# Kernel tuning notes

Hardware: AMD Instinct MI355X
Metric: run time of the kernel (lower is better)

## Reference

```python
import jax, jax.numpy as jnp
import numpy as np

B, T, D, U, N = 32, 2048, 128, 512, 256
THETA = 1000.0


def _lmu_AT_BT(order, theta):
    # Legendre delay state-space (Voelker LMU), then ZOH discretization (dt=1).
    q = np.arange(order, dtype=np.float32)
    r = (2.0 * q + 1.0) / np.float32(theta)
    i, j = np.meshgrid(q, q, indexing='ij')
    A = np.where(i < j, -1.0, (-1.0) ** (i - j + 1)).astype(np.float32) * r[:, None]
    Bv = ((-1.0) ** q).astype(np.float32) * r
    # ZOH via augmented matrix exponential: expm([[A, B],[0, 0]])
    M = np.zeros((order + 1, order + 1), np.float32)
    M[:order, :order] = A
    M[:order, order] = Bv
    eM = jax.scipy.linalg.expm(jnp.asarray(M))
    Ad = eM[:order, :order]
    Bd = eM[:order, order:order + 1]
    AT = (Ad - jnp.eye(order, dtype=jnp.float32)).T  # (A_d - I)^T, [N,N]
    BT = Bd.T  # [1,N]
    return AT, BT


def setup_inputs() -> dict:
    key = jax.random.key(0)
    ks = jax.random.split(key, 6)
    AT, BT = _lmu_AT_BT(N, THETA)
    return {
        'x': jax.random.normal(ks[0], (B, T, D), jnp.float32),
        'h0': jnp.zeros((B, U), jnp.float32),
        'm0': jnp.zeros((B, N), jnp.float32),
        'input_encoders': jax.random.normal(ks[1], (D, 1), jnp.float32) / jnp.sqrt(jnp.float32(D)),
        'hidden_encoders': jax.random.normal(ks[2], (U, 1), jnp.float32) / jnp.sqrt(jnp.float32(U)),
        'memory_encoders': jnp.zeros((N, 1), jnp.float32),
        'input_kernel': jax.random.normal(ks[3], (D, U), jnp.float32) / jnp.sqrt(jnp.float32(D)),
        'hidden_kernel': jax.random.normal(ks[4], (U, U), jnp.float32) / jnp.sqrt(jnp.float32(U)),
        'memory_kernel': jax.random.normal(ks[5], (N, U), jnp.float32) / jnp.sqrt(jnp.float32(N)),
        'AT': AT,
        'BT': BT,
    }


def reference(x, h0, m0, input_encoders, hidden_encoders, memory_encoders,
              input_kernel, hidden_kernel, memory_kernel, AT, BT):
    # Precompute input projections for all timesteps (parallel GEMMs).
    ux = jnp.einsum('btd,de->bte', x, input_encoders)     # [B,T,1]
    xk = jnp.einsum('btd,du->btu', x, input_kernel)       # [B,T,U]

    def step(carry, inp):
        h, m = carry
        ux_t, xk_t = inp
        u = ux_t + h @ hidden_encoders + m @ memory_encoders  # [B,1]
        m = m + m @ AT + u @ BT                               # [B,N]
        h = jnp.tanh(xk_t + h @ hidden_kernel + m @ memory_kernel)  # [B,U]
        return (h, m), h

    xs = (ux.transpose(1, 0, 2), xk.transpose(1, 0, 2))  # time-major
    (_, _), hs = jax.lax.scan(step, (h0, m0), xs)
    return hs.transpose(1, 0, 2)  # [B,T,U]
```

## Files before the change

kernel.cpp:

```cpp
#include <hip/hip_runtime.h>
#include <math.h>

#define T_LEN 2048
#define B_SZ  32
#define D_IN  128
#define U_SZ  512
#define N_SZ  256
#define GS    64
#define NT    512

constexpr size_t OFF_AM  = 0;
constexpr size_t OFF_WMM = OFF_AM  + (size_t)N_SZ*N_SZ;
constexpr size_t OFF_BW  = OFF_WMM + (size_t)N_SZ*U_SZ;
constexpr size_t OFF_UX  = OFF_BW  + U_SZ;
constexpr size_t OFF_XT  = OFF_UX  + (size_t)T_LEN*B_SZ;
constexpr size_t OFF_S   = OFF_XT  + (size_t)T_LEN*D_IN*B_SZ;
constexpr size_t OFF_FLG = OFF_S   + (size_t)2*768*B_SZ;

#define FMA4(A, S0, W0) \
  A.x = fmaf(S0, W0.x, A.x); A.y = fmaf(S0, W0.y, A.y); \
  A.z = fmaf(S0, W0.z, A.z); A.w = fmaf(S0, W0.w, A.w);

__device__ inline float2 ld_agent_f2(const float* p) {
  unsigned long long v = __hip_atomic_load((const unsigned long long*)p,
                                           __ATOMIC_RELAXED, __HIP_MEMORY_SCOPE_AGENT);
  union { unsigned long long u; float2 f; } c; c.u = v; return c.f;
}
__device__ inline void st_agent_f1(float* p, float f) {
  union { float f; unsigned u; } c; c.f = f;
  __hip_atomic_store((unsigned*)p, c.u, __ATOMIC_RELAXED, __HIP_MEMORY_SCOPE_AGENT);
}

__global__ void k_am(const float* __restrict__ AT, const float* __restrict__ me,
                     const float* __restrict__ BT, float* __restrict__ ws) {
  int k = blockIdx.x, j = threadIdx.x;
  float v = AT[(size_t)k*N_SZ + j] + (k == j ? 1.0f : 0.0f) + me[k]*BT[j];
  ws[OFF_AM + (size_t)k*N_SZ + j] = v;
}

__global__ void k_bw(const float* __restrict__ BT, const float* __restrict__ Wm,
                     float* __restrict__ ws) {
  int j = blockIdx.x*256 + threadIdx.x;
  float acc = 0.f;
  for (int q = 0; q < N_SZ; ++q) acc += BT[q]*Wm[(size_t)q*U_SZ + j];
  ws[OFF_BW + j] = acc;
}

__global__ void k_wmm(const float* __restrict__ Wm, float* __restrict__ ws) {
  __shared__ float amr[N_SZ];
  int k = blockIdx.x, tid = threadIdx.x;
  amr[tid] = ws[OFF_AM + (size_t)k*N_SZ + tid];
  __syncthreads();
  float acc0 = 0.f, acc1 = 0.f;
  for (int q = 0; q < N_SZ; ++q) {
    float a = amr[q];
    acc0 += a * Wm[(size_t)q*U_SZ + tid];
    acc1 += a * Wm[(size_t)q*U_SZ + tid + 256];
  }
  ws[OFF_WMM + (size_t)k*U_SZ + tid]       = acc0;
  ws[OFF_WMM + (size_t)k*U_SZ + tid + 256] = acc1;
}

__global__ void k_ux(const float* __restrict__ x, const float* __restrict__ ie,
                     float* __restrict__ ws) {
  __shared__ __align__(16) float iel[D_IN];
  __shared__ float red[B_SZ*9];
  int t = blockIdx.x, tid = threadIdx.x;
  if (tid < D_IN) iel[tid] = ie[tid];
  __syncthreads();
  int b = tid >> 3, p = tid & 7;
  const float4* xr = (const float4*)(x + ((size_t)b*T_LEN + t)*D_IN);
  const float4* wr = (const float4*)iel;
  float s = 0.f;
  for (int q = 0; q < 4; ++q) {
    int fi = p + q*8;
    float4 v = xr[fi];
    float4 w = wr[fi];
    s += v.x*w.x + v.y*w.y + v.z*w.z + v.w*w.w;
  }
  red[b*9 + p] = s;
  __syncthreads();
  if (tid < B_SZ) {
    float acc = 0.f;
    for (int p2 = 0; p2 < 8; ++p2) acc += red[tid*9 + p2];
    ws[OFF_UX + (size_t)t*B_SZ + tid] = acc;
  }
}

__global__ void k_xt(const float* __restrict__ x, float* __restrict__ ws) {
  __shared__ float tile[B_SZ*33];
  int bid = blockIdx.x;
  int t = bid >> 2, d0 = (bid & 3)*32;
  int tid = threadIdx.x;
  int lo = tid & 31, hi = tid >> 5;
  for (int p = 0; p < 4; ++p) {
    int b = hi + p*8;
    tile[b*33 + lo] = x[((size_t)b*T_LEN + t)*D_IN + d0 + lo];
  }
  __syncthreads();
  float* dst = ws + OFF_XT + ((size_t)t*D_IN + d0)*B_SZ;
  for (int p = 0; p < 4; ++p) {
    int d = hi + p*8;
    dst[(size_t)d*B_SZ + lo] = tile[lo*33 + d];
  }
}

__global__ void k_init(const float* __restrict__ h0, const float* __restrict__ mm0,
                       float* __restrict__ ws) {
  int bid = blockIdx.x, tid = threadIdx.x;
  if (bid < 24) {
    for (int i = 0; i < 4; ++i) {
      int e = bid*1024 + i*256 + tid;
      int k = e >> 5, b = e & 31;
      float v = (k < U_SZ) ? h0[(size_t)b*U_SZ + k] : mm0[(size_t)b*N_SZ + (k - U_SZ)];
      ws[OFF_S + e] = v;
    }
  } else {
    for (int idx = tid; idx < GS*16; idx += 256) ws[OFF_FLG + idx] = 0.0f;
  }
}

__global__ __launch_bounds__(NT, 2) void k_scan(
    const float* __restrict__ Wh, const float* __restrict__ Wi,
    const float* __restrict__ he, const float* __restrict__ btv,
    float* __restrict__ ws, float* __restrict__ out)
{
  const int g = blockIdx.x, tid = threadIdx.x;
  const int JH = g*8, JM = g*4;
  const int bt = tid & 7, jt = (tid >> 3) & 1, ks = tid >> 4;
  const int b0 = bt*4;

  float* uxw = ws + OFF_UX;
  float* xT  = ws + OFF_XT;
  float* Sb  = ws + OFF_S;
  unsigned* flags = (unsigned*)(ws + OFF_FLG);

  __shared__ __align__(16) float Wl[896*8];
  __shared__ __align__(16) float Aml[N_SZ*4];
  __shared__ float Hl[U_SZ];
  __shared__ float redh[NT*17];
  __shared__ float redm[256*17];
  __shared__ float reds[256*9];
  __shared__ float bwl[8], btl[4];

  for (int idx = tid; idx < 896*8; idx += NT) {
    int k = idx >> 3, jj = idx & 7;
    float v;
    if (k < 512)      v = Wh[(size_t)k*U_SZ + JH + jj];
    else if (k < 768) v = ws[OFF_WMM + (size_t)(k-512)*U_SZ + JH + jj];
    else              v = Wi[(size_t)(k-768)*U_SZ + JH + jj];
    Wl[idx] = v;
  }
  for (int idx = tid; idx < N_SZ*4; idx += NT) {
    int k = idx >> 2, jj = idx & 3;
    Aml[idx] = ws[OFF_AM + (size_t)k*N_SZ + JM + jj];
  }
  for (int idx = tid; idx < U_SZ; idx += NT) Hl[idx] = he[idx];
  if (tid < 8) bwl[tid] = ws[OFF_BW + JH + tid];
  if (tid < 4) btl[tid] = btv[JM + tid];
  __syncthreads();

  const float4* Wl4  = (const float4*)Wl;
  const float4* Aml4 = (const float4*)Aml;

  float4 a0={0,0,0,0}, a1={0,0,0,0}, a2={0,0,0,0}, a3={0,0,0,0};
  {
    const float* xrow = xT;
    #pragma unroll
    for (int i = 24; i < 28; ++i) {
      int kk = i*32 + ks;
      float4 sv = *(const float4*)(xrow + (size_t)(kk - 768)*B_SZ + b0);
      float4 wv = Wl4[kk*2 + jt];
      FMA4(a0, sv.x, wv) FMA4(a1, sv.y, wv) FMA4(a2, sv.z, wv) FMA4(a3, sv.w, wv)
    }
  }

  for (int t = 0; t < T_LEN; ++t) {
    const float* S  = Sb + (size_t)(t & 1)*(768*B_SZ);
    float*       Sn = Sb + (size_t)((t+1) & 1)*(768*B_SZ);

    float uxv = uxw[(size_t)t*B_SZ + (tid & 31)];

    float4 q0={0,0,0,0}, q1={0,0,0,0}, q2={0,0,0,0}, q3={0,0,0,0};
    float4 sa={0,0,0,0};

    #pragma unroll 8
    for (int i = 0; i < 16; ++i) {
      int kk = i*32 + ks;
      const float* sp0 = S + (size_t)kk*B_SZ + b0;
      float2 s01 = ld_agent_f2(sp0);
      float2 s23 = ld_agent_f2(sp0 + 2);
      float4 wv = Wl4[kk*2 + jt];
      float hv = Hl[kk];
      FMA4(a0, s01.x, wv) FMA4(a1, s01.y, wv) FMA4(a2, s23.x, wv) FMA4(a3, s23.y, wv)
      sa.x = fmaf(s01.x, hv, sa.x); sa.y = fmaf(s01.y, hv, sa.y);
      sa.z = fmaf(s23.x, hv, sa.z); sa.w = fmaf(s23.y, hv, sa.w);
    }
    #pragma unroll 8
    for (int i = 16; i < 24; ++i) {
      int kk = i*32 + ks;
      const float* sp0 = S + (size_t)kk*B_SZ + b0;
      float2 s01 = ld_agent_f2(sp0);
      float2 s23 = ld_agent_f2(sp0 + 2);
      float4 wv = Wl4[kk*2 + jt];
      FMA4(a0, s01.x, wv) FMA4(a1, s01.y, wv) FMA4(a2, s23.x, wv) FMA4(a3, s23.y, wv)
      float4 av = Aml4[kk - 512];
      FMA4(q0, s01.x, av) FMA4(q1, s01.y, av) FMA4(q2, s23.x, av) FMA4(q3, s23.y, av)
    }

    {
      float* rp = redh + tid*17;
      rp[0]=a0.x;  rp[1]=a0.y;  rp[2]=a0.z;  rp[3]=a0.w;
      rp[4]=a1.x;  rp[5]=a1.y;  rp[6]=a1.z;  rp[7]=a1.w;
      rp[8]=a2.x;  rp[9]=a2.y;  rp[10]=a2.z; rp[11]=a2.w;
      rp[12]=a3.x; rp[13]=a3.y; rp[14]=a3.z; rp[15]=a3.w;
      if (jt == 0) {
        int idx = bt + 8*ks;
        float* rm = redm + idx*17;
        rm[0]=q0.x;  rm[1]=q0.y;  rm[2]=q0.z;  rm[3]=q0.w;
        rm[4]=q1.x;  rm[5]=q1.y;  rm[6]=q1.z;  rm[7]=q1.w;
        rm[8]=q2.x;  rm[9]=q2.y;  rm[10]=q2.z; rm[11]=q2.w;
        rm[12]=q3.x; rm[13]=q3.y; rm[14]=q3.z; rm[15]=q3.w;
        float* rs = reds + idx*9;
        rs[0]=sa.x; rs[1]=sa.y; rs[2]=sa.z; rs[3]=sa.w;
      }
    }
    __syncthreads();

    float val = 0.f;
    if (tid < 384) {
      const int be2 = tid & 31, btb = be2 >> 2, xx = be2 & 3;
      float ssb = uxv;
      #pragma unroll
      for (int k2 = 0; k2 < 32; ++k2) ssb += reds[(btb + 8*k2)*9 + xx];
      if (tid < 256) {
        const int je = tid >> 5, jt2 = je >> 2, yy = je & 3;
        float sum = 0.f;
        #pragma unroll
        for (int k2 = 0; k2 < 32; ++k2)
          sum += redh[(btb + 8*jt2 + 16*k2)*17 + xx*4 + yy];
        val = tanhf(sum + ssb*bwl[je]);
        st_agent_f1(Sn + (size_t)(JH + je)*B_SZ + be2, val);
      } else {
        const int jm = (tid - 256) >> 5;
        float sum = 0.f;
        #pragma unroll
        for (int k2 = 0; k2 < 32; ++k2)
          sum += redm[(btb + 8*k2)*17 + xx*4 + jm];
        sum += ssb*btl[jm];
        st_agent_f1(Sn + (size_t)(512 + JM + jm)*B_SZ + be2, sum);
      }
    }
    __syncthreads();

    if (t + 1 < T_LEN && tid == 0)
      __hip_atomic_store(flags + (size_t)g*16, (unsigned)(t + 1),
                         __ATOMIC_RELAXED, __HIP_MEMORY_SCOPE_AGENT);
    if (tid < 256)
      out[((size_t)(tid & 31)*T_LEN + t)*U_SZ + JH + (tid >> 5)] = val;

    a0.x=a0.y=a0.z=a0.w=0.f; a1=a0; a2=a0; a3=a0;
    if (t + 1 < T_LEN) {
      const float* xrow = xT + (size_t)(t+1)*D_IN*B_SZ;
      #pragma unroll
      for (int i = 24; i < 28; ++i) {
        int kk = i*32 + ks;
        float4 sv = *(const float4*)(xrow + (size_t)(kk - 768)*B_SZ + b0);
        float4 wv = Wl4[kk*2 + jt];
        FMA4(a0, sv.x, wv) FMA4(a1, sv.y, wv) FMA4(a2, sv.z, wv) FMA4(a3, sv.w, wv)
      }
      if (tid < 64) {
        const unsigned* fp = flags + (size_t)tid*16;
        while (__hip_atomic_load(fp, __ATOMIC_RELAXED, __HIP_MEMORY_SCOPE_AGENT)
               < (unsigned)(t + 1)) { }
      }
    }
    __syncthreads();
  }
}

extern "C" void kernel_launch(void* const* d_in, const int* in_sizes, int n_in,
                              void* d_out, int out_size, void* d_ws, size_t ws_size,
                              hipStream_t stream) {
  const float* x   = (const float*)d_in[0];
  const float* h0  = (const float*)d_in[1];
  const float* m0  = (const float*)d_in[2];
  const float* ie  = (const float*)d_in[3];
  const float* he  = (const float*)d_in[4];
  const float* me  = (const float*)d_in[5];
  const float* Wi  = (const float*)d_in[6];
  const float* Wh  = (const float*)d_in[7];
  const float* Wm  = (const float*)d_in[8];
  const float* AT  = (const float*)d_in[9];
  const float* BT  = (const float*)d_in[10];
  float* ws  = (float*)d_ws;
  float* out = (float*)d_out;

  k_am  <<<N_SZ, 256, 0, stream>>>(AT, me, BT, ws);
  k_bw  <<<2, 256, 0, stream>>>(BT, Wm, ws);
  k_wmm <<<N_SZ, 256, 0, stream>>>(Wm, ws);
  k_ux  <<<T_LEN, 256, 0, stream>>>(x, ie, ws);
  k_xt  <<<T_LEN*4, 256, 0, stream>>>(x, ws);
  k_init<<<25, 256, 0, stream>>>(h0, m0, ws);
  k_scan<<<GS, NT, 0, stream>>>(Wh, Wi, he, BT, ws, out);
}
```

Before: 11.41 ms.

## Split batch into two halves with separate flags to pipeline the recurrent scan

Each timestep is split into two half-batch sub-steps of 16 rows each, and each half gets its own set of cross-block progress flags. While one half waits on the grid-wide flag barrier, the other half's work can proceed, which is meant to hide inter-block synchronisation latency. Threads are remapped so all 512 cover the smaller batch slice, with doubled reduction depth. The cost is twice as many barriers and reduction passes per timestep, each doing half the work.

Result: slower. 15.19 ms (+33.2%).

```diff
diff --git a/kernel.cpp b/kernel.cpp
--- a/kernel.cpp
+++ b/kernel.cpp
@@ -20,6 +20,8 @@
 #define FMA4(A, S0, W0) \
   A.x = fmaf(S0, W0.x, A.x); A.y = fmaf(S0, W0.y, A.y); \
   A.z = fmaf(S0, W0.z, A.z); A.w = fmaf(S0, W0.w, A.w);
+#define FMA2(A, S0, W0) \
+  A.x = fmaf(S0, W0.x, A.x); A.y = fmaf(S0, W0.y, A.y);
 
 __device__ inline float2 ld_agent_f2(const float* p) {
   unsigned long long v = __hip_atomic_load((const unsigned long long*)p,
@@ -116,7 +118,7 @@
       ws[OFF_S + e] = v;
     }
   } else {
-    for (int idx = tid; idx < GS*16; idx += 256) ws[OFF_FLG + idx] = 0.0f;
+    for (int idx = tid; idx < 2*GS*16; idx += 256) ws[OFF_FLG + idx] = 0.0f;
   }
 }
 
@@ -127,7 +129,7 @@
 {
   const int g = blockIdx.x, tid = threadIdx.x;
   const int JH = g*8, JM = g*4;
-  const int bt = tid & 7, jt = (tid >> 3) & 1, ks = tid >> 4;
+  const int bt = tid & 3, jt = (tid >> 2) & 1, ks = tid >> 3;
   const int b0 = bt*4;
 
   float* uxw = ws + OFF_UX;
@@ -139,7 +141,7 @@
   __shared__ __align__(16) float Aml[N_SZ*4];
   __shared__ float Hl[U_SZ];
   __shared__ float redh[NT*17];
-  __shared__ float redm[256*17];
+  __shared__ float redm[NT*9];
   __shared__ float reds[256*9];
   __shared__ float bwl[8], btl[4];
 
@@ -161,33 +163,35 @@
   __syncthreads();
 
   const float4* Wl4  = (const float4*)Wl;
-  const float4* Aml4 = (const float4*)Aml;
+  const float2* Aml2 = (const float2*)Aml;
 
   float4 a0={0,0,0,0}, a1={0,0,0,0}, a2={0,0,0,0}, a3={0,0,0,0};
   {
     const float* xrow = xT;
     #pragma unroll
-    for (int i = 24; i < 28; ++i) {
-      int kk = i*32 + ks;
+    for (int i = 0; i < 2; ++i) {
+      int kk = 768 + i*64 + ks;
       float4 sv = *(const float4*)(xrow + (size_t)(kk - 768)*B_SZ + b0);
       float4 wv = Wl4[kk*2 + jt];
       FMA4(a0, sv.x, wv) FMA4(a1, sv.y, wv) FMA4(a2, sv.z, wv) FMA4(a3, sv.w, wv)
     }
   }
 
-  for (int t = 0; t < T_LEN; ++t) {
+  for (int cc = 0; cc < 2*T_LEN; ++cc) {
+    const int t = cc >> 1, c = cc & 1, g16 = c << 4;
     const float* S  = Sb + (size_t)(t & 1)*(768*B_SZ);
     float*       Sn = Sb + (size_t)((t+1) & 1)*(768*B_SZ);
-
-    float uxv = uxw[(size_t)t*B_SZ + (tid & 31)];
-
-    float4 q0={0,0,0,0}, q1={0,0,0,0}, q2={0,0,0,0}, q3={0,0,0,0};
+    const int boff = g16 + b0;
+
+    float uxv = uxw[(size_t)t*B_SZ + g16 + (tid & 15)];
+
+    float2 q0={0,0}, q1={0,0}, q2={0,0}, q3={0,0};
     float4 sa={0,0,0,0};
 
-    #pragma unroll 8
-    for (int i = 0; i < 16; ++i) {
-      int kk = i*32 + ks;
-      const float* sp0 = S + (size_t)kk*B_SZ + b0;
+    #pragma unroll
+    for (int i = 0; i < 8; ++i) {
+      int kk = i*64 + ks;
+      const float* sp0 = S + (size_t)kk*B_SZ + boff;
       float2 s01 = ld_agent_f2(sp0);
       float2 s23 = ld_agent_f2(sp0 + 2);
       float4 wv = Wl4[kk*2 + jt];
@@ -196,16 +200,16 @@
       sa.x = fmaf(s01.x, hv, sa.x); sa.y = fmaf(s01.y, hv, sa.y);
       sa.z = fmaf(s23.x, hv, sa.z); sa.w = fmaf(s23.y, hv, sa.w);
     }
-    #pragma unroll 8
-    for (int i = 16; i < 24; ++i) {
-      int kk = i*32 + ks;
-      const float* sp0 = S + (size_t)kk*B_SZ + b0;
+    #pragma unroll
+    for (int i = 0; i < 4; ++i) {
+      int kk = 512 + i*64 + ks;
+      const float* sp0 = S + (size_t)kk*B_SZ + boff;
       float2 s01 = ld_agent_f2(sp0);
       float2 s23 = ld_agent_f2(sp0 + 2);
       float4 wv = Wl4[kk*2 + jt];
       FMA4(a0, s01.x, wv) FMA4(a1, s01.y, wv) FMA4(a2, s23.x, wv) FMA4(a3, s23.y, wv)
-      float4 av = Aml4[kk - 512];
-      FMA4(q0, s01.x, av) FMA4(q1, s01.y, av) FMA4(q2, s23.x, av) FMA4(q3, s23.y, av)
+      float2 av = Aml2[(kk - 512)*2 + jt];
+      FMA2(q0, s01.x, av) FMA2(q1, s01.y, av) FMA2(q2, s23.x, av) FMA2(q3, s23.y, av)
     }
 
     {
@@ -214,65 +218,65 @@
       rp[4]=a1.x;  rp[5]=a1.y;  rp[6]=a1.z;  rp[7]=a1.w;
       rp[8]=a2.x;  rp[9]=a2.y;  rp[10]=a2.z; rp[11]=a2.w;
       rp[12]=a3.x; rp[13]=a3.y; rp[14]=a3.z; rp[15]=a3.w;
+      float* rm = redm + tid*9;
+      rm[0]=q0.x; rm[1]=q0.y; rm[2]=q1.x; rm[3]=q1.y;
+      rm[4]=q2.x; rm[5]=q2.y; rm[6]=q3.x; rm[7]=q3.y;
       if (jt == 0) {
-        int idx = bt + 8*ks;
-        float* rm = redm + idx*17;
-        rm[0]=q0.x;  rm[1]=q0.y;  rm[2]=q0.z;  rm[3]=q0.w;
-        rm[4]=q1.x;  rm[5]=q1.y;  rm[6]=q1.z;  rm[7]=q1.w;
-        rm[8]=q2.x;  rm[9]=q2.y;  rm[10]=q2.z; rm[11]=q2.w;
-        rm[12]=q3.x; rm[13]=q3.y; rm[14]=q3.z; rm[15]=q3.w;
-        float* rs = reds + idx*9;
+        float* rs = reds + (bt + 4*ks)*9;
         rs[0]=sa.x; rs[1]=sa.y; rs[2]=sa.z; rs[3]=sa.w;
       }
     }
     __syncthreads();
 
     float val = 0.f;
-    if (tid < 384) {
-      const int be2 = tid & 31, btb = be2 >> 2, xx = be2 & 3;
+    if (tid < 192) {
+      const int be2 = tid & 15, btb = be2 >> 2, xx = be2 & 3;
       float ssb = uxv;
       #pragma unroll
-      for (int k2 = 0; k2 < 32; ++k2) ssb += reds[(btb + 8*k2)*9 + xx];
-      if (tid < 256) {
-        const int je = tid >> 5, jt2 = je >> 2, yy = je & 3;
+      for (int k2 = 0; k2 < 64; ++k2) ssb += reds[(btb + 4*k2)*9 + xx];
+      if (tid < 128) {
+        const int je = tid >> 4, jt2 = je >> 2, yy = je & 3;
         float sum = 0.f;
         #pragma unroll
-        for (int k2 = 0; k2 < 32; ++k2)
-          sum += redh[(btb + 8*jt2 + 16*k2)*17 + xx*4 + yy];
+        for (int k2 = 0; k2 < 64; ++k2)
+          sum += redh[(btb + 4*jt2 + 8*k2)*17 + xx*4 + yy];
         val = tanhf(sum + ssb*bwl[je]);
-        st_agent_f1(Sn + (size_t)(JH + je)*B_SZ + be2, val);
+        st_agent_f1(Sn + (size_t)(JH + je)*B_SZ + g16 + be2, val);
       } else {
-        const int jm = (tid - 256) >> 5;
+        const int jm = (tid - 128) >> 4;
+        const int jtm = jm >> 1, jc = jm & 1;
         float sum = 0.f;
         #pragma unroll
-        for (int k2 = 0; k2 < 32; ++k2)
-          sum += redm[(btb + 8*k2)*17 + xx*4 + jm];
+        for (int k2 = 0; k2 < 64; ++k2)
+          sum += redm[(btb + 4*jtm + 8*k2)*9 + xx*2 + jc];
         sum += ssb*btl[jm];
-        st_agent_f1(Sn + (size_t)(512 + JM + jm)*B_SZ + be2, sum);
+        st_agent_f1(Sn + (size_t)(512 + JM + jm)*B_SZ + g16 + be2, sum);
       }
     }
     __syncthreads();
 
+    const int cn = cc + 1, t2 = cn >> 1, c2 = cn & 1;
     if (t + 1 < T_LEN && tid == 0)
-      __hip_atomic_store(flags + (size_t)g*16, (unsigned)(t + 1),
+      __hip_atomic_store(flags + ((size_t)c*GS + g)*16, (unsigned)(t + 1),
                          __ATOMIC_RELAXED, __HIP_MEMORY_SCOPE_AGENT);
-    if (tid < 256)
-      out[((size_t)(tid & 31)*T_LEN + t)*U_SZ + JH + (tid >> 5)] = val;
+    if (tid < 128)
+      out[((size_t)(g16 + (tid & 15))*T_LEN + t)*U_SZ + JH + (tid >> 4)] = val;
 
     a0.x=a0.y=a0.z=a0.w=0.f; a1=a0; a2=a0; a3=a0;
-    if (t + 1 < T_LEN) {
-      const float* xrow = xT + (size_t)(t+1)*D_IN*B_SZ;
+    if (cn < 2*T_LEN) {
+      const int g16n = c2 << 4;
+      const float* xrow = xT + (size_t)t2*D_IN*B_SZ;
       #pragma unroll
-      for (int i = 24; i < 28; ++i) {
-        int kk = i*32 + ks;
-        float4 sv = *(const float4*)(xrow + (size_t)(kk - 768)*B_SZ + b0);
+      for (int i = 0; i < 2; ++i) {
+        int kk = 768 + i*64 + ks;
+        float4 sv = *(const float4*)(xrow + (size_t)(kk - 768)*B_SZ + g16n + b0);
         float4 wv = Wl4[kk*2 + jt];
         FMA4(a0, sv.x, wv) FMA4(a1, sv.y, wv) FMA4(a2, sv.z, wv) FMA4(a3, sv.w, wv)
       }
-      if (tid < 64) {
-        const unsigned* fp = flags + (size_t)tid*16;
+      if (tid < GS) {
+        const unsigned* fp = flags + ((size_t)c2*GS + tid)*16;
         while (__hip_atomic_load(fp, __ATOMIC_RELAXED, __HIP_MEMORY_SCOPE_AGENT)
-               < (unsigned)(t + 1)) { }
+               < (unsigned)t2) { }
       }
     }
     __syncthreads();
```
